# Kernel optimization log

Measured on AMD Instinct MI355X. Metric: run time of the kernel, lower is better.

Reference implementation:

```python
import jax, jax.numpy as jnp
import numpy as np

V, E, H, M = 256, 512, 512, 128
D = 2 * H  # decoder hidden
B, L_TXT, T_MEL = 32, 256, 800
EPS = 1e-5


def setup_inputs() -> dict:
    key = jax.random.key(0)
    ks = jax.random.split(key, 24)
    s = 0.02
    inp = {
        'x': jax.random.randint(ks[0], (B, L_TXT), 0, V),
        'text_seq_lens': jax.random.randint(ks[1], (B,), 1, L_TXT + 1),
        'y': jax.random.normal(ks[2], (B, T_MEL, M), jnp.float32),
        'mel_spec_lens': jax.random.randint(ks[3], (B,), 1, T_MEL + 1),
        'emb': jax.random.normal(ks[4], (V, E)) * s,
        'conv1_w': jax.random.normal(ks[5], (E, E, 3)) * s,
        'conv1_b': jnp.zeros((E,)),
        'bn1_g': jnp.ones((E,)), 'bn1_b': jnp.zeros((E,)),
        'conv2_w': jax.random.normal(ks[6], (E, E, 3)) * s,
        'conv2_b': jnp.zeros((E,)),
        'bn2_g': jnp.ones((E,)), 'bn2_b': jnp.zeros((E,)),
        'wih_f': jax.random.normal(ks[7], (4 * H, E)) * s,
        'whh_f': jax.random.normal(ks[8], (4 * H, H)) * s,
        'bih_f': jnp.zeros((4 * H,)), 'bhh_f': jnp.zeros((4 * H,)),
        'wih_b': jax.random.normal(ks[9], (4 * H, E)) * s,
        'whh_b': jax.random.normal(ks[10], (4 * H, H)) * s,
        'bih_b': jnp.zeros((4 * H,)), 'bhh_b': jnp.zeros((4 * H,)),
        'dwih': jax.random.normal(ks[11], (4 * D, M)) * s,
        'dwhh': jax.random.normal(ks[12], (4 * D, D)) * s,
        'dbih': jnp.zeros((4 * D,)), 'dbhh': jnp.zeros((4 * D,)),
        'proj_w': jax.random.normal(ks[13], (M, D)) * s,
        'proj_b': jnp.zeros((M,)),
        'gate_w': jax.random.normal(ks[14], (1, D)) * s,
        'gate_b': jnp.zeros((1,)),
    }
    return inp


def _conv_bn_relu(x, w, b, g, beta):
    # x: (B, E, L); training-mode BatchNorm (batch statistics, biased var)
    x = jax.lax.conv_general_dilated(x, w, (1,), [(1, 1)],
                                     dimension_numbers=('NCH', 'OIH', 'NCH')) + b[None, :, None]
    mu = jnp.mean(x, axis=(0, 2), keepdims=True)
    var = jnp.mean((x - mu) ** 2, axis=(0, 2), keepdims=True)
    x = (x - mu) * jax.lax.rsqrt(var + EPS) * g[None, :, None] + beta[None, :, None]
    return jax.nn.relu(x)


def _lstm_last(xseq, lens, wih, whh, bih, bhh):
    # Run LSTM over full padded seq, freezing state past each length.
    # Returns final (h, c) == state at t = len-1 (packed-sequence semantics).
    Bb, T, _ = xseq.shape
    Hh = whh.shape[1]
    pre = jnp.einsum('bte,ge->btg', xseq, wih) + bih + bhh  # (B,T,4H)

    def step(carry, inp):
        h, c = carry
        xt, t = inp
        gates = xt + h @ whh.T
        i, f, g, o = jnp.split(gates, 4, axis=-1)
        c_n = jax.nn.sigmoid(f) * c + jax.nn.sigmoid(i) * jnp.tanh(g)
        h_n = jax.nn.sigmoid(o) * jnp.tanh(c_n)
        valid = (t < lens)[:, None]
        return (jnp.where(valid, h_n, h), jnp.where(valid, c_n, c)), None

    init = (jnp.zeros((Bb, Hh), xseq.dtype), jnp.zeros((Bb, Hh), xseq.dtype))
    (h, c), _ = jax.lax.scan(step, init, (pre.transpose(1, 0, 2), jnp.arange(T)))
    return h, c


def _forward(x, text_seq_lens, y, mel_spec_lens, emb, conv1_w, conv1_b, bn1_g, bn1_b,
             conv2_w, conv2_b, bn2_g, bn2_b, wih_f, whh_f, bih_f, bhh_f,
             wih_b, whh_b, bih_b, bhh_b, dwih, dwhh, dbih, dbhh,
             proj_w, proj_b, gate_w, gate_b):
    xe = emb[x]                       # (B, L, E)
    h = xe.transpose(0, 2, 1)         # (B, E, L)
    h = _conv_bn_relu(h, conv1_w, conv1_b, bn1_g, bn1_b)  # dropout = identity (eval)
    h = _conv_bn_relu(h, conv2_w, conv2_b, bn2_g, bn2_b)
    h = h.transpose(0, 2, 1)          # (B, L, E)

    # bidirectional encoder LSTM final states (packed semantics)
    hf, cf = _lstm_last(h, text_seq_lens, wih_f, whh_f, bih_f, bhh_f)
    # reverse each sequence within its valid length for the backward direction
    t_idx = jnp.arange(h.shape[1])[None, :]
    rev_idx = jnp.clip(text_seq_lens[:, None] - 1 - t_idx, 0, h.shape[1] - 1)
    h_rev = jnp.take_along_axis(h, rev_idx[:, :, None], axis=1)
    hb, cb = _lstm_last(h_rev, text_seq_lens, wih_b, whh_b, bih_b, bhh_b)

    hid = jnp.concatenate([hf, hb], axis=1)  # (B, 2H)
    cel = jnp.concatenate([cf, cb], axis=1)

    Tm = y.shape[1]

    def dec_step(carry, _):
        hd, cd, inp = carry
        gates = inp @ dwih.T + dbih + dbhh + hd @ dwhh.T
        i, f, g, o = jnp.split(gates, 4, axis=-1)
        cd = jax.nn.sigmoid(f) * cd + jax.nn.sigmoid(i) * jnp.tanh(g)
        hd = jax.nn.sigmoid(o) * jnp.tanh(cd)
        mel = hd @ proj_w.T + proj_b          # (B, M)
        gate = hd @ gate_w.T + gate_b         # (B, 1)
        return (hd, cd, mel), (mel, gate[:, 0])

    sos = jnp.zeros((y.shape[0], M), y.dtype)
    _, (mels, gates) = jax.lax.scan(dec_step, (hid, cel, sos), None, length=Tm)
    mel_outputs = mels.transpose(1, 0, 2)     # (B, Tm, M)
    gate_outputs = gates.T                    # (B, Tm)

    mask = jnp.arange(Tm)[None, :] > mel_spec_lens[:, None]  # (B, Tm), strictly >
    masked_mel = jnp.where(mask[:, :, None], 0.0, mel_outputs)
    masked_gate = jnp.where(mask, 1000.0, gate_outputs)
    return masked_mel, masked_gate, mask


def reference(x, text_seq_lens, y, mel_spec_lens, emb, conv1_w, conv1_b, bn1_g, bn1_b,
              conv2_w, conv2_b, bn2_g, bn2_b, wih_f, whh_f, bih_f, bhh_f,
              wih_b, whh_b, bih_b, bhh_b, dwih, dwhh, dbih, dbhh,
              proj_w, proj_b, gate_w, gate_b):
    return _forward(x, text_seq_lens, y, mel_spec_lens, emb, conv1_w, conv1_b,
                    bn1_g, bn1_b, conv2_w, conv2_b, bn2_g, bn2_b,
                    wih_f, whh_f, bih_f, bhh_f, wih_b, whh_b, bih_b, bhh_b,
                    dwih, dwhh, dbih, dbhh, proj_w, proj_b, gate_w, gate_b)
```

## Files before the change

kernel.cpp:

```cpp
#include <hip/hip_runtime.h>


typedef float f4 __attribute__((ext_vector_type(4)));
typedef _Float16 h8 __attribute__((ext_vector_type(8)));
typedef _Float16 half_t;
typedef unsigned long long u64;

#define B_    32
#define LTXT  256
#define TMEL  800
#define EE    512
#define HH    512
#define DD    1024
#define MM    128
#define NROWS 8192
#define GATE_OFF 3276800
#define MASK_OFF 3302400

#define RING_D 801
#define RING_E 257
#define HOP    13

#define WS_MBE        0ull
#define WS_MBD        16384ull
#define WS_HENC       49152ull
#define WS_ZERO_BYTES 114688ull
#define WS_HD         16891904ull
#define WS_BUFX       69386240ull
#define WS_BUFY       77774848ull
#define WS_CONVF      86163456ull
#define WS_WEFF       86163456ull
#define WS_W0         94552064ull
#define WS_WP1        102940672ull
#define WS_WP2        104513536ull
#define WS_WIHP       106086400ull
#define WS_WHHP       110280704ull
#define WS_BSUM       114475008ull
#define WS_BEFF       114491392ull
#define WS_B0         114507776ull
#define WS_MEAN       114524160ull
#define WS_RSTD       114526208ull
#define WS_PROJW      114528256ull
#define WS_PROJG      114790400ull
#define WS_CEL        114823168ull

__device__ __forceinline__ float sigm(float x) { return 1.f / (1.f + __expf(-x)); }
__device__ __forceinline__ float tanh_f(float x) {
    float e = __expf(2.f * x);
    return 1.f - 2.f / (e + 1.f);
}

__device__ __forceinline__ void st_atom64(void* p, u64 v) {
    asm volatile("global_atomic_swap_x2 %0, %1, off" :: "v"(p), "v"(v) : "memory");
}
__device__ __forceinline__ void st_atom32(unsigned* p, unsigned v) {
    asm volatile("global_atomic_swap %0, %1, off" :: "v"(p), "v"(v) : "memory");
}


__global__ void k_embed(const int* __restrict__ x, const float* __restrict__ emb,
                        half_t* __restrict__ out) {
    int row = blockIdx.x;
    int tok = x[row];
    const float* e = emb + (size_t)tok * EE;
    half_t* o = out + (size_t)row * EE;
    for (int c = threadIdx.x; c < EE; c += blockDim.x) o[c] = (half_t)e[c];
}

__global__ void k_packconvw(const float* __restrict__ w, half_t* __restrict__ wp) {
    int idx = blockIdx.x * 256 + threadIdx.x;
    if (idx >= 3 * EE * EE) return;
    int s = idx / (EE * EE);
    int rem = idx - s * EE * EE;
    int eo = rem >> 9, ei = rem & 511;
    wp[idx] = (half_t)w[(size_t)eo * (EE * 3) + ei * 3 + s];
}

__global__ __launch_bounds__(256) void k_conv(const half_t* __restrict__ A,
                                              const half_t* __restrict__ Wp,
                                              const float* __restrict__ bias,
                                              float* __restrict__ out) {
    const int nt = blockIdx.x, et = blockIdx.y;
    const int tid = threadIdx.x;
    const int wv = tid >> 6, l = tid & 63, quad = l >> 4, lo = l & 15;
    const int rowA = nt * 64 + wv * 16 + lo;
    const int eo = et * 16 + lo;
    f4 acc = {0.f, 0.f, 0.f, 0.f};
    for (int s = 0; s < 3; ++s) {
        int lsp = (rowA & 255) + s - 1;
        bool valid = (lsp >= 0) && (lsp < 256);
        int rs = rowA + s - 1;
        rs = rs < 0 ? 0 : (rs > NROWS - 1 ? NROWS - 1 : rs);
        const half_t* ab = A + (size_t)rs * EE;
        const half_t* wb = Wp + ((size_t)s * EE + eo) * EE;
#pragma unroll 4
        for (int ks = 0; ks < 16; ++ks) {
            h8 a = {0, 0, 0, 0, 0, 0, 0, 0};
            if (valid) a = *(const h8*)(ab + ks * 32 + quad * 8);
            h8 b = *(const h8*)(wb + ks * 32 + quad * 8);
            acc = __builtin_amdgcn_mfma_f32_16x16x32_f16(a, b, acc, 0, 0, 0);
        }
    }
    const int orow = nt * 64 + wv * 16 + quad * 4;
    const float bv = bias[eo];
#pragma unroll
    for (int r = 0; r < 4; ++r) out[(size_t)(orow + r) * EE + eo] = acc[r] + bv;
}

__global__ __launch_bounds__(256) void k_bnstats(const float* __restrict__ x,
                                                 float* __restrict__ mean,
                                                 float* __restrict__ rstd) {
    const int c = blockIdx.x;
    float s = 0.f, ss = 0.f;
    for (int n = threadIdx.x; n < NROWS; n += 256) {
        float v = x[(size_t)n * EE + c];
        s += v; ss += v * v;
    }
#pragma unroll
    for (int off = 32; off > 0; off >>= 1) { s += __shfl_down(s, off); ss += __shfl_down(ss, off); }
    __shared__ float as[4], ass[4];
    int wv = threadIdx.x >> 6;
    if ((threadIdx.x & 63) == 0) { as[wv] = s; ass[wv] = ss; }
    __syncthreads();
    if (threadIdx.x == 0) {
        float S = as[0] + as[1] + as[2] + as[3];
        float SS = ass[0] + ass[1] + ass[2] + ass[3];
        float m = S / (float)NROWS;
        float var = SS / (float)NROWS - m * m;
        mean[c] = m;
        rstd[c] = rsqrtf(var + 1e-5f);
    }
}

__global__ void k_bnapply(const float* __restrict__ x, const float* __restrict__ mean,
                          const float* __restrict__ rstd, const float* __restrict__ g,
                          const float* __restrict__ beta, half_t* __restrict__ out) {
    int idx = blockIdx.x * 256 + threadIdx.x;
    if (idx >= NROWS * EE) return;
    int c = idx & (EE - 1);
    float v = (x[idx] - mean[c]) * rstd[c] * g[c] + beta[c];
    out[idx] = (half_t)(v > 0.f ? v : 0.f);
}

__global__ void k_packrec(const float* __restrict__ src, half_t* __restrict__ dst,
                          int Hdim, int kshift, int total) {
    int idx = blockIdx.x * 256 + threadIdx.x;
    if (idx >= total) return;
    int p = idx >> kshift;
    int k = idx & ((1 << kshift) - 1);
    int he = p >> 2, g = p & 3;
    dst[idx] = (half_t)src[((size_t)g * Hdim + he) * (size_t)(1 << kshift) + k];
}

__global__ void k_bsumenc(const float* __restrict__ bf, const float* __restrict__ bhf,
                          const float* __restrict__ bb, const float* __restrict__ bhb,
                          float* __restrict__ bsum) {
    int p = blockIdx.x * 256 + threadIdx.x;
    if (p >= 4096) return;
    int dir = p >> 11, pp = p & 2047;
    int he = pp >> 2, g = pp & 3;
    int row = g * HH + he;
    bsum[p] = dir ? (bb[row] + bhb[row]) : (bf[row] + bhf[row]);
}

__global__ __launch_bounds__(256) void k_weff(const float* __restrict__ dwhh,
                                              const float* __restrict__ dwih,
                                              const float* __restrict__ projw,
                                              half_t* __restrict__ weff,
                                              half_t* __restrict__ w0) {
    int row = blockIdx.x;
    int k = blockIdx.y * 256 + threadIdx.x;
    float v = dwhh[(size_t)row * DD + k];
    float acc = v;
    for (int m = 0; m < MM; ++m) acc += dwih[(size_t)row * MM + m] * projw[(size_t)m * DD + k];
    int p = ((row & (DD - 1)) << 2) | (row >> 10);
    weff[(size_t)p * DD + k] = (half_t)acc;
    w0[(size_t)p * DD + k] = (half_t)v;
}

__global__ void k_bdec(const float* __restrict__ dbih, const float* __restrict__ dbhh,
                       const float* __restrict__ dwih, const float* __restrict__ projb,
                       float* __restrict__ beff, float* __restrict__ b0) {
    int p = blockIdx.x * 256 + threadIdx.x;
    if (p >= 4096) return;
    int he = p >> 2, g = p & 3;
    int row = g * DD + he;
    float bb = dbih[row] + dbhh[row];
    float acc = bb;
    for (int m = 0; m < MM; ++m) acc += dwih[(size_t)row * MM + m] * projb[m];
    b0[p] = bb;
    beff[p] = acc;
}

__global__ void k_cast(const float* __restrict__ src, half_t* __restrict__ dst, int n) {
    int idx = blockIdx.x * 256 + threadIdx.x;
    if (idx < n) dst[idx] = (half_t)src[idx];
}

__global__ void k_projg(const float* __restrict__ gw, half_t* __restrict__ pg) {
    int idx = blockIdx.x * 256 + threadIdx.x;
    if (idx >= 16 * DD) return;
    int row = idx >> 10, k = idx & (DD - 1);
    pg[idx] = (half_t)(row == 0 ? gw[k] : 0.f);
}

__global__ void k_mask(const int* __restrict__ lens, float* __restrict__ out) {
    int idx = blockIdx.x * 256 + threadIdx.x;
    if (idx >= B_ * TMEL) return;
    int b = idx / TMEL, t = idx - b * TMEL;
    out[MASK_OFF + idx] = (t > lens[b]) ? 1.f : 0.f;
}

__global__ __launch_bounds__(512) void k_enc(const half_t* __restrict__ X,
                                             const half_t* __restrict__ wihp,
                                             const half_t* __restrict__ whhp,
                                             const float* __restrict__ bsum,
                                             const int* __restrict__ lens,
                                             half_t* __restrict__ henc,
                                             half_t* __restrict__ hd,
                                             float* __restrict__ cel,
                                             unsigned* __restrict__ mbE) {
    const int j = blockIdx.x;
    const int d = j >> 4, jj = j & 15;
    const int dir = d >> 1, bg = d & 1;
    const int tid = threadIdx.x;
    const int wv = tid >> 6, l = tid & 63, quad = l >> 4, lo = l & 15;
    const int ue = tid >> 4;
    const int ub = tid & 15;

    __shared__ half_t s_hd[16 * 520];
    __shared__ float s_g[16][129];
    __shared__ float s_c[32][16];
    __shared__ float s_h[32][16];
    __shared__ half_t s_hh[32][16];
    __shared__ int s_len[16];

    if (tid < 16) s_len[tid] = lens[bg * 16 + tid];
    s_c[ue][ub] = 0.f;
    s_h[ue][ub] = 0.f;

    const int pr = dir * 2048 + jj * 128 + wv * 16 + lo;
    const half_t* wih_b = wihp + (size_t)pr * 512;
    const half_t* whh_b = whhp + (size_t)pr * 512;
    const float bias_n = bsum[pr];

    h8 wihreg[16], whhreg[16];
#pragma unroll
    for (int ks = 0; ks < 16; ++ks) {
        wihreg[ks] = *(const h8*)(wih_b + ks * 32 + quad * 8);
        whhreg[ks] = *(const h8*)(whh_b + ks * 32 + quad * 8);
    }

    int sp = 0, sn = HOP;
    __syncthreads();

    for (int t = 0; t < 256; ++t) {
        if (t > 0) {
            if (wv == 1 && l < 16) {
                const unsigned want = (unsigned)t;
                const unsigned* fp = mbE + (size_t)(d * 16 + jj) * 64 + l;
                while (__hip_atomic_load(fp, __ATOMIC_RELAXED, __HIP_MEMORY_SCOPE_AGENT) < want)
                    __builtin_amdgcn_s_sleep(1);
            }
            __syncthreads();
        }

        const half_t* src = henc + ((size_t)sp * 4 + d) * 8192;
        h8 tmp0 = *(const h8*)(src + (size_t)(tid + 0 * 512) * 8);
        h8 tmp1 = *(const h8*)(src + (size_t)(tid + 1 * 512) * 8);

        const int lb = s_len[lo];
        int tt = (dir == 0) ? t : (lb - 1 - t);
        tt = tt < 0 ? 0 : tt;
        const half_t* xr = X + ((size_t)(bg * 16 + lo) * 256 + tt) * 512;
        f4 accA = {0.f, 0.f, 0.f, 0.f}, accB = {0.f, 0.f, 0.f, 0.f};
#pragma unroll
        for (int ks = 0; ks < 16; ++ks) {
            h8 a = *(const h8*)(xr + ks * 32 + quad * 8);
            accA = __builtin_amdgcn_mfma_f32_16x16x32_f16(a, wihreg[ks], accA, 0, 0, 0);
        }

        {
            int c0 = tid;
            *(h8*)(s_hd + (size_t)(c0 >> 6) * 520 + (c0 & 63) * 8) = tmp0;
            int c1 = tid + 512;
            *(h8*)(s_hd + (size_t)(c1 >> 6) * 520 + (c1 & 63) * 8) = tmp1;
        }
        __syncthreads();

        const half_t* ar = s_hd + (size_t)lo * 520 + quad * 8;
#pragma unroll
        for (int ks = 0; ks < 16; ++ks) {
            h8 a = *(const h8*)(ar + ks * 32);
            accB = __builtin_amdgcn_mfma_f32_16x16x32_f16(a, whhreg[ks], accB, 0, 0, 0);
        }
#pragma unroll
        for (int r = 0; r < 4; ++r) s_g[quad * 4 + r][wv * 16 + lo] = accA[r] + accB[r] + bias_n;
        __syncthreads();
        {
            float gi = s_g[ub][ue * 4 + 0], gf = s_g[ub][ue * 4 + 1];
            float gg = s_g[ub][ue * 4 + 2], go = s_g[ub][ue * 4 + 3];
            float cn = sigm(gf) * s_c[ue][ub] + sigm(gi) * tanh_f(gg);
            float hn = sigm(go) * tanh_f(cn);
            if (t < s_len[ub]) { s_c[ue][ub] = cn; s_h[ue][ub] = hn; }
            s_hh[ue][ub] = (half_t)s_h[ue][ub];
        }
        __syncthreads();
        if (tid < 64 && t < 255) {
            int b2 = tid >> 2, e8 = (tid & 3) * 8;
            union { half_t h[8]; u64 u[2]; } pk;
#pragma unroll
            for (int i = 0; i < 8; ++i) pk.h[i] = s_hh[e8 + i][b2];
            half_t* dst = henc + ((size_t)sn * 4 + d) * 8192 + (size_t)b2 * 512 + jj * 32 + e8;
            st_atom64(dst, pk.u[0]);
            st_atom64(dst + 4, pk.u[1]);
            asm volatile("s_waitcnt vmcnt(0)");
            if (tid < 16)
                st_atom32(mbE + ((size_t)(d * 16 + tid) * 64 + jj), (unsigned)(t + 1));
        }
        if (t < 255) { sp = sn; sn += HOP; if (sn >= RING_E) sn -= RING_E; }
    }
    hd[(size_t)bg * ((size_t)RING_D * 16384) + (size_t)ub * 1024
       + dir * 512 + jj * 32 + ue] = (half_t)s_h[ue][ub];
    cel[(size_t)(bg * 16 + ub) * 1024 + dir * 512 + jj * 32 + ue] = s_c[ue][ub];
}

__global__ __launch_bounds__(512) void k_dec(const half_t* __restrict__ Weff,
                                             const half_t* __restrict__ W0,
                                             const float* __restrict__ beff,
                                             const float* __restrict__ b0,
                                             const half_t* __restrict__ projwb,
                                             const half_t* __restrict__ projg,
                                             const float* __restrict__ projb,
                                             const float* __restrict__ gateb,
                                             const int* __restrict__ mlens,
                                             const float* __restrict__ cel,
                                             half_t* __restrict__ hd,
                                             float* __restrict__ out,
                                             unsigned* __restrict__ mbD) {
    const int j = blockIdx.x;
    const int tid = threadIdx.x;
    const int wv = tid >> 6, l = tid & 63, quad = l >> 4, lo = l & 15;

    __shared__ half_t s_hd[16 * 1032];
    __shared__ float s_g[16][129];
    __shared__ float s_c[32][16];
    __shared__ half_t s_hh[32][16];
    __shared__ int s_len[32];

    if (j < 64) {
        const int g = j >> 5, jj = j & 31;
        half_t* hdG = hd + (size_t)g * ((size_t)RING_D * 16384);
        unsigned* mbG = mbD + (size_t)g * 34 * 64;
        const int ue = tid >> 4;
        const int ub = tid & 15;

        s_c[ue][ub] = cel[(size_t)(g * 16 + ub) * 1024 + jj * 32 + ue];
        const int pr = jj * 128 + wv * 16 + lo;
        const float biasE = beff[pr], bias0 = b0[pr];
        const half_t* wbE = Weff + (size_t)pr * 1024;
        const half_t* wb0 = W0 + (size_t)pr * 1024;

        h8 wreg[32];
#pragma unroll
        for (int ks = 0; ks < 32; ++ks)
            wreg[ks] = *(const h8*)(wbE + ks * 32 + quad * 8);

        int sp = 0, sn = HOP;
        __syncthreads();

        for (int t = 1; t <= TMEL; ++t) {
            if (t > 1) {
                if (tid >= 64 && tid < 96) {
                    const unsigned want = (unsigned)(t - 1);
                    const unsigned* fp = mbG + (size_t)jj * 64 + (tid - 64);
                    while (__hip_atomic_load(fp, __ATOMIC_RELAXED, __HIP_MEMORY_SCOPE_AGENT) < want)
                        __builtin_amdgcn_s_sleep(1);
                }
                __syncthreads();
            }

            {
                const half_t* src = hdG + (size_t)sp * 16384;
                h8 tp[4];
#pragma unroll
                for (int i = 0; i < 4; ++i)
                    tp[i] = *(const h8*)(src + (size_t)(tid + i * 512) * 8);
#pragma unroll
                for (int i = 0; i < 4; ++i) {
                    int c = tid + i * 512;
                    *(h8*)(s_hd + (size_t)(c >> 7) * 1032 + (c & 127) * 8) = tp[i];
                }
            }
            __syncthreads();

            const half_t* ar = s_hd + (size_t)lo * 1032 + quad * 8;
            f4 acc = {0.f, 0.f, 0.f, 0.f}, acc2 = {0.f, 0.f, 0.f, 0.f};
            if (t == 1) {
#pragma unroll 8
                for (int ks = 0; ks < 32; ks += 2) {
                    h8 a0 = *(const h8*)(ar + ks * 32);
                    h8 a1 = *(const h8*)(ar + ks * 32 + 32);
                    acc = __builtin_amdgcn_mfma_f32_16x16x32_f16(a0, *(const h8*)(wb0 + ks * 32 + quad * 8), acc, 0, 0, 0);
                    acc2 = __builtin_amdgcn_mfma_f32_16x16x32_f16(a1, *(const h8*)(wb0 + ks * 32 + 32 + quad * 8), acc2, 0, 0, 0);
                }
            } else {
#pragma unroll
                for (int ks = 0; ks < 32; ks += 2) {
                    h8 a0 = *(const h8*)(ar + ks * 32);
                    h8 a1 = *(const h8*)(ar + ks * 32 + 32);
                    acc = __builtin_amdgcn_mfma_f32_16x16x32_f16(a0, wreg[ks], acc, 0, 0, 0);
                    acc2 = __builtin_amdgcn_mfma_f32_16x16x32_f16(a1, wreg[ks + 1], acc2, 0, 0, 0);
                }
            }
            const float bn = (t == 1) ? bias0 : biasE;
#pragma unroll
            for (int r = 0; r < 4; ++r) s_g[quad * 4 + r][wv * 16 + lo] = acc[r] + acc2[r] + bn;
            __syncthreads();
            {
                float gi = s_g[ub][ue * 4 + 0], gf = s_g[ub][ue * 4 + 1];
                float gg = s_g[ub][ue * 4 + 2], go = s_g[ub][ue * 4 + 3];
                float cn = sigm(gf) * s_c[ue][ub] + sigm(gi) * tanh_f(gg);
                s_c[ue][ub] = cn;
                s_hh[ue][ub] = (half_t)(sigm(go) * tanh_f(cn));
            }
            __syncthreads();
            if (tid < 64) {
                int b2 = tid >> 2, e8 = (tid & 3) * 8;
                union { half_t h[8]; u64 u[2]; } pk;
#pragma unroll
                for (int i = 0; i < 8; ++i) pk.h[i] = s_hh[e8 + i][b2];
                half_t* dst = hdG + (size_t)sn * 16384 + (size_t)b2 * 1024 + jj * 32 + e8;
                st_atom64(dst, pk.u[0]);
                st_atom64(dst + 4, pk.u[1]);
                asm volatile("s_waitcnt vmcnt(0)");
                if (tid < 34)
                    st_atom32(mbG + ((size_t)tid * 64 + jj), (unsigned)t);
            }
            sp = sn; sn += HOP; if (sn >= RING_D) sn -= RING_D;
        }
    } else {
        const int p = j - 64;
        const int g = p >> 1;
        const bool meld = ((p & 1) == 0);
        half_t* hdG = hd + (size_t)g * ((size_t)RING_D * 16384);
        unsigned* mbG = mbD + (size_t)g * 34 * 64;
        const int cons = meld ? 32 : 33;
        const bool duty = meld || (wv == 0);
        const half_t* pw = meld ? (projwb + (size_t)(wv * 16 + lo) * 1024)
                                : (projg + (size_t)lo * 1024);
        const float biasP = meld ? projb[wv * 16 + lo] : gateb[0];

        h8 pwreg[32];
        if (duty) {
#pragma unroll
            for (int ks = 0; ks < 32; ++ks)
                pwreg[ks] = *(const h8*)(pw + ks * 32 + quad * 8);
        }
        if (tid < 32) s_len[tid] = mlens[tid];

        int spP = HOP;
        __syncthreads();

        for (int t = 1; t <= TMEL; ++t) {
            if (tid < 32) {
                const unsigned want = (unsigned)t;
                const unsigned* fp = mbG + (size_t)cons * 64 + tid;
                while (__hip_atomic_load(fp, __ATOMIC_RELAXED, __HIP_MEMORY_SCOPE_AGENT) < want)
                    __builtin_amdgcn_s_sleep(1);
            }
            __syncthreads();

            {
                const half_t* src = hdG + (size_t)spP * 16384;
                h8 tp[4];
#pragma unroll
                for (int i = 0; i < 4; ++i)
                    tp[i] = *(const h8*)(src + (size_t)(tid + i * 512) * 8);
#pragma unroll
                for (int i = 0; i < 4; ++i) {
                    int c = tid + i * 512;
                    *(h8*)(s_hd + (size_t)(c >> 7) * 1032 + (c & 127) * 8) = tp[i];
                }
            }
            __syncthreads();

            if (duty) {
                const half_t* ar = s_hd + (size_t)lo * 1032 + quad * 8;
                f4 accm = {0.f, 0.f, 0.f, 0.f}, accm2 = {0.f, 0.f, 0.f, 0.f};
#pragma unroll
                for (int ks = 0; ks < 32; ks += 2) {
                    h8 a0 = *(const h8*)(ar + ks * 32);
                    h8 a1 = *(const h8*)(ar + ks * 32 + 32);
                    accm = __builtin_amdgcn_mfma_f32_16x16x32_f16(a0, pwreg[ks], accm, 0, 0, 0);
                    accm2 = __builtin_amdgcn_mfma_f32_16x16x32_f16(a1, pwreg[ks + 1], accm2, 0, 0, 0);
                }
                accm[0] += accm2[0]; accm[1] += accm2[1];
                accm[2] += accm2[2]; accm[3] += accm2[3];
                const int pos = t - 1;
                if (meld) {
#pragma unroll
                    for (int r = 0; r < 4; ++r) {
                        int b = g * 16 + quad * 4 + r;
                        float v = accm[r] + biasP;
                        if (pos > s_len[b]) v = 0.f;
                        __builtin_nontemporal_store(v,
                            &out[(size_t)b * (TMEL * MM) + (size_t)pos * MM + wv * 16 + lo]);
                    }
                } else if (lo == 0) {
#pragma unroll
                    for (int r = 0; r < 4; ++r) {
                        int b = g * 16 + quad * 4 + r;
                        float v = accm[r] + biasP;
                        if (pos > s_len[b]) v = 1000.f;
                        __builtin_nontemporal_store(v, &out[GATE_OFF + (size_t)b * TMEL + pos]);
                    }
                }
            }
            __syncthreads();
            spP += HOP; if (spP >= RING_D) spP -= RING_D;
        }
    }
}


extern "C" void kernel_launch(void* const* d_in, const int* in_sizes, int n_in,
                              void* d_out, int out_size, void* d_ws, size_t ws_size,
                              hipStream_t stream) {
    const int* x = (const int*)d_in[0];
    const int* tlens = (const int*)d_in[1];
    const int* mlens = (const int*)d_in[3];
    const float* emb = (const float*)d_in[4];
    const float* c1w = (const float*)d_in[5];
    const float* c1b = (const float*)d_in[6];
    const float* bn1g = (const float*)d_in[7];
    const float* bn1b = (const float*)d_in[8];
    const float* c2w = (const float*)d_in[9];
    const float* c2b = (const float*)d_in[10];
    const float* bn2g = (const float*)d_in[11];
    const float* bn2b = (const float*)d_in[12];
    const float* wihf = (const float*)d_in[13];
    const float* whhf = (const float*)d_in[14];
    const float* bihf = (const float*)d_in[15];
    const float* bhhf = (const float*)d_in[16];
    const float* wihb = (const float*)d_in[17];
    const float* whhb = (const float*)d_in[18];
    const float* bihb = (const float*)d_in[19];
    const float* bhhb = (const float*)d_in[20];
    const float* dwih = (const float*)d_in[21];
    const float* dwhh = (const float*)d_in[22];
    const float* dbih = (const float*)d_in[23];
    const float* dbhh = (const float*)d_in[24];
    const float* projw = (const float*)d_in[25];
    const float* projb = (const float*)d_in[26];
    const float* gatew = (const float*)d_in[27];
    const float* gateb = (const float*)d_in[28];
    float* out = (float*)d_out;
    char* ws = (char*)d_ws;

    unsigned* mbE = (unsigned*)(ws + WS_MBE);
    unsigned* mbD = (unsigned*)(ws + WS_MBD);
    half_t* henc = (half_t*)(ws + WS_HENC);
    half_t* hd = (half_t*)(ws + WS_HD);
    half_t* bufX = (half_t*)(ws + WS_BUFX);
    half_t* bufY = (half_t*)(ws + WS_BUFY);
    float* convf = (float*)(ws + WS_CONVF);
    half_t* weff = (half_t*)(ws + WS_WEFF);
    half_t* w0 = (half_t*)(ws + WS_W0);
    half_t* wp1 = (half_t*)(ws + WS_WP1);
    half_t* wp2 = (half_t*)(ws + WS_WP2);
    float* meanb = (float*)(ws + WS_MEAN);
    float* rstdb = (float*)(ws + WS_RSTD);
    half_t* wihp = (half_t*)(ws + WS_WIHP);
    half_t* whhp = (half_t*)(ws + WS_WHHP);
    float* bsum = (float*)(ws + WS_BSUM);
    float* beff = (float*)(ws + WS_BEFF);
    float* b0 = (float*)(ws + WS_B0);
    half_t* projwb = (half_t*)(ws + WS_PROJW);
    half_t* projg = (half_t*)(ws + WS_PROJG);
    float* cel = (float*)(ws + WS_CEL);

    hipMemsetAsync(d_ws, 0, (size_t)WS_ZERO_BYTES, stream);

    k_embed<<<NROWS, 256, 0, stream>>>(x, emb, bufX);
    k_packconvw<<<(3 * EE * EE + 255) / 256, 256, 0, stream>>>(c1w, wp1);
    k_conv<<<dim3(128, 32), 256, 0, stream>>>(bufX, wp1, c1b, convf);
    k_bnstats<<<EE, 256, 0, stream>>>(convf, meanb, rstdb);
    k_bnapply<<<(NROWS * EE) / 256, 256, 0, stream>>>(convf, meanb, rstdb, bn1g, bn1b, bufY);
    k_packconvw<<<(3 * EE * EE + 255) / 256, 256, 0, stream>>>(c2w, wp2);
    k_conv<<<dim3(128, 32), 256, 0, stream>>>(bufY, wp2, c2b, convf);
    k_bnstats<<<EE, 256, 0, stream>>>(convf, meanb, rstdb);
    k_bnapply<<<(NROWS * EE) / 256, 256, 0, stream>>>(convf, meanb, rstdb, bn2g, bn2b, bufX);

    const int encTot = 2048 * 512;
    k_packrec<<<(encTot + 255) / 256, 256, 0, stream>>>(wihf, wihp, HH, 9, encTot);
    k_packrec<<<(encTot + 255) / 256, 256, 0, stream>>>(wihb, wihp + encTot, HH, 9, encTot);
    k_packrec<<<(encTot + 255) / 256, 256, 0, stream>>>(whhf, whhp, HH, 9, encTot);
    k_packrec<<<(encTot + 255) / 256, 256, 0, stream>>>(whhb, whhp + encTot, HH, 9, encTot);
    k_bsumenc<<<16, 256, 0, stream>>>(bihf, bhhf, bihb, bhhb, bsum);

    k_enc<<<64, 512, 0, stream>>>(bufX, wihp, whhp, bsum, tlens, henc, hd, cel, mbE);

    k_weff<<<dim3(4096, 4), 256, 0, stream>>>(dwhh, dwih, projw, weff, w0);
    k_bdec<<<16, 256, 0, stream>>>(dbih, dbhh, dwih, projb, beff, b0);
    k_cast<<<(MM * DD + 255) / 256, 256, 0, stream>>>(projw, projwb, MM * DD);
    k_projg<<<(16 * DD + 255) / 256, 256, 0, stream>>>(gatew, projg);

    k_dec<<<68, 512, 0, stream>>>(weff, w0, beff, b0, projwb, projg, projb, gateb,
                                  mlens, cel, hd, out, mbD);

    k_mask<<<(B_ * TMEL + 255) / 256, 256, 0, stream>>>(mlens, out);

    (void)in_sizes; (void)n_in; (void)out_size; (void)ws_size;
}
```

Before: 4.464 ms.

## Fuse encoder, decoder and weight prep into one persistent kernel with counters

```diff
diff --git a/kernel.cpp b/kernel.cpp
--- a/kernel.cpp
+++ b/kernel.cpp
@@ -20,9 +20,13 @@
 #define RING_D 801
 #define RING_E 257
 #define HOP    13
+#define ENCTOT 1048576
+#define PREPN  60
+#define ENCN   64
 
 #define WS_MBE        0ull
 #define WS_MBD        16384ull
+#define WS_CNT        40960ull
 #define WS_HENC       49152ull
 #define WS_ZERO_BYTES 114688ull
 #define WS_HD         16891904ull
@@ -53,8 +57,14 @@
 __device__ __forceinline__ void st_atom64(void* p, u64 v) {
     asm volatile("global_atomic_swap_x2 %0, %1, off" :: "v"(p), "v"(v) : "memory");
 }
-__device__ __forceinline__ void st_atom32(unsigned* p, unsigned v) {
+__device__ __forceinline__ void st_atom32(void* p, unsigned v) {
     asm volatile("global_atomic_swap %0, %1, off" :: "v"(p), "v"(v) : "memory");
+}
+__device__ __forceinline__ void st_wt32(void* p, unsigned v) {
+    asm volatile("global_store_dword %0, %1, off sc0 sc1" :: "v"(p), "v"(v) : "memory");
+}
+__device__ __forceinline__ unsigned f2u(float f) {
+    union { float f; unsigned u; } c; c.f = f; return c.u;
 }
 
 
@@ -142,214 +152,251 @@
     out[idx] = (half_t)(v > 0.f ? v : 0.f);
 }
 
-__global__ void k_packrec(const float* __restrict__ src, half_t* __restrict__ dst,
-                          int Hdim, int kshift, int total) {
-    int idx = blockIdx.x * 256 + threadIdx.x;
-    if (idx >= total) return;
-    int p = idx >> kshift;
-    int k = idx & ((1 << kshift) - 1);
-    int he = p >> 2, g = p & 3;
-    dst[idx] = (half_t)src[((size_t)g * Hdim + he) * (size_t)(1 << kshift) + k];
-}
-
-__global__ void k_bsumenc(const float* __restrict__ bf, const float* __restrict__ bhf,
-                          const float* __restrict__ bb, const float* __restrict__ bhb,
-                          float* __restrict__ bsum) {
-    int p = blockIdx.x * 256 + threadIdx.x;
-    if (p >= 4096) return;
-    int dir = p >> 11, pp = p & 2047;
-    int he = pp >> 2, g = pp & 3;
-    int row = g * HH + he;
-    bsum[p] = dir ? (bb[row] + bhb[row]) : (bf[row] + bhf[row]);
-}
-
-__global__ __launch_bounds__(256) void k_weff(const float* __restrict__ dwhh,
-                                              const float* __restrict__ dwih,
-                                              const float* __restrict__ projw,
-                                              half_t* __restrict__ weff,
-                                              half_t* __restrict__ w0) {
-    int row = blockIdx.x;
-    int k = blockIdx.y * 256 + threadIdx.x;
-    float v = dwhh[(size_t)row * DD + k];
-    float acc = v;
-    for (int m = 0; m < MM; ++m) acc += dwih[(size_t)row * MM + m] * projw[(size_t)m * DD + k];
-    int p = ((row & (DD - 1)) << 2) | (row >> 10);
-    weff[(size_t)p * DD + k] = (half_t)acc;
-    w0[(size_t)p * DD + k] = (half_t)v;
-}
-
-__global__ void k_bdec(const float* __restrict__ dbih, const float* __restrict__ dbhh,
-                       const float* __restrict__ dwih, const float* __restrict__ projb,
-                       float* __restrict__ beff, float* __restrict__ b0) {
-    int p = blockIdx.x * 256 + threadIdx.x;
-    if (p >= 4096) return;
-    int he = p >> 2, g = p & 3;
-    int row = g * DD + he;
-    float bb = dbih[row] + dbhh[row];
-    float acc = bb;
-    for (int m = 0; m < MM; ++m) acc += dwih[(size_t)row * MM + m] * projb[m];
-    b0[p] = bb;
-    beff[p] = acc;
-}
-
-__global__ void k_cast(const float* __restrict__ src, half_t* __restrict__ dst, int n) {
-    int idx = blockIdx.x * 256 + threadIdx.x;
-    if (idx < n) dst[idx] = (half_t)src[idx];
-}
-
-__global__ void k_projg(const float* __restrict__ gw, half_t* __restrict__ pg) {
-    int idx = blockIdx.x * 256 + threadIdx.x;
-    if (idx >= 16 * DD) return;
-    int row = idx >> 10, k = idx & (DD - 1);
-    pg[idx] = (half_t)(row == 0 ? gw[k] : 0.f);
-}
-
-__global__ void k_mask(const int* __restrict__ lens, float* __restrict__ out) {
-    int idx = blockIdx.x * 256 + threadIdx.x;
-    if (idx >= B_ * TMEL) return;
-    int b = idx / TMEL, t = idx - b * TMEL;
-    out[MASK_OFF + idx] = (t > lens[b]) ? 1.f : 0.f;
-}
-
-__global__ __launch_bounds__(512) void k_enc(const half_t* __restrict__ X,
-                                             const half_t* __restrict__ wihp,
-                                             const half_t* __restrict__ whhp,
-                                             const float* __restrict__ bsum,
-                                             const int* __restrict__ lens,
-                                             half_t* __restrict__ henc,
-                                             half_t* __restrict__ hd,
-                                             float* __restrict__ cel,
-                                             unsigned* __restrict__ mbE) {
-    const int j = blockIdx.x;
-    const int d = j >> 4, jj = j & 15;
-    const int dir = d >> 1, bg = d & 1;
-    const int tid = threadIdx.x;
-    const int wv = tid >> 6, l = tid & 63, quad = l >> 4, lo = l & 15;
-    const int ue = tid >> 4;
-    const int ub = tid & 15;
-
-    __shared__ half_t s_hd[16 * 520];
-    __shared__ float s_g[16][129];
-    __shared__ float s_c[32][16];
-    __shared__ float s_h[32][16];
-    __shared__ half_t s_hh[32][16];
-    __shared__ int s_len[16];
-
-    if (tid < 16) s_len[tid] = lens[bg * 16 + tid];
-    s_c[ue][ub] = 0.f;
-    s_h[ue][ub] = 0.f;
-
-    const int pr = dir * 2048 + jj * 128 + wv * 16 + lo;
-    const half_t* wih_b = wihp + (size_t)pr * 512;
-    const half_t* whh_b = whhp + (size_t)pr * 512;
-    const float bias_n = bsum[pr];
-
-    h8 wihreg[16], whhreg[16];
-#pragma unroll
-    for (int ks = 0; ks < 16; ++ks) {
-        wihreg[ks] = *(const h8*)(wih_b + ks * 32 + quad * 8);
-        whhreg[ks] = *(const h8*)(whh_b + ks * 32 + quad * 8);
-    }
-
-    int sp = 0, sn = HOP;
-    __syncthreads();
-
-    for (int t = 0; t < 256; ++t) {
-        if (t > 0) {
-            if (wv == 1 && l < 16) {
-                const unsigned want = (unsigned)t;
-                const unsigned* fp = mbE + (size_t)(d * 16 + jj) * 64 + l;
-                while (__hip_atomic_load(fp, __ATOMIC_RELAXED, __HIP_MEMORY_SCOPE_AGENT) < want)
-                    __builtin_amdgcn_s_sleep(1);
-            }
-            __syncthreads();
-        }
-
-        const half_t* src = henc + ((size_t)sp * 4 + d) * 8192;
-        h8 tmp0 = *(const h8*)(src + (size_t)(tid + 0 * 512) * 8);
-        h8 tmp1 = *(const h8*)(src + (size_t)(tid + 1 * 512) * 8);
-
-        const int lb = s_len[lo];
-        int tt = (dir == 0) ? t : (lb - 1 - t);
-        tt = tt < 0 ? 0 : tt;
-        const half_t* xr = X + ((size_t)(bg * 16 + lo) * 256 + tt) * 512;
-        f4 accA = {0.f, 0.f, 0.f, 0.f}, accB = {0.f, 0.f, 0.f, 0.f};
-#pragma unroll
-        for (int ks = 0; ks < 16; ++ks) {
-            h8 a = *(const h8*)(xr + ks * 32 + quad * 8);
-            accA = __builtin_amdgcn_mfma_f32_16x16x32_f16(a, wihreg[ks], accA, 0, 0, 0);
-        }
-
-        {
-            int c0 = tid;
-            *(h8*)(s_hd + (size_t)(c0 >> 6) * 520 + (c0 & 63) * 8) = tmp0;
-            int c1 = tid + 512;
-            *(h8*)(s_hd + (size_t)(c1 >> 6) * 520 + (c1 & 63) * 8) = tmp1;
-        }
-        __syncthreads();
-
-        const half_t* ar = s_hd + (size_t)lo * 520 + quad * 8;
-#pragma unroll
-        for (int ks = 0; ks < 16; ++ks) {
-            h8 a = *(const h8*)(ar + ks * 32);
-            accB = __builtin_amdgcn_mfma_f32_16x16x32_f16(a, whhreg[ks], accB, 0, 0, 0);
-        }
-#pragma unroll
-        for (int r = 0; r < 4; ++r) s_g[quad * 4 + r][wv * 16 + lo] = accA[r] + accB[r] + bias_n;
-        __syncthreads();
-        {
-            float gi = s_g[ub][ue * 4 + 0], gf = s_g[ub][ue * 4 + 1];
-            float gg = s_g[ub][ue * 4 + 2], go = s_g[ub][ue * 4 + 3];
-            float cn = sigm(gf) * s_c[ue][ub] + sigm(gi) * tanh_f(gg);
-            float hn = sigm(go) * tanh_f(cn);
-            if (t < s_len[ub]) { s_c[ue][ub] = cn; s_h[ue][ub] = hn; }
-            s_hh[ue][ub] = (half_t)s_h[ue][ub];
-        }
-        __syncthreads();
-        if (tid < 64 && t < 255) {
-            int b2 = tid >> 2, e8 = (tid & 3) * 8;
-            union { half_t h[8]; u64 u[2]; } pk;
-#pragma unroll
-            for (int i = 0; i < 8; ++i) pk.h[i] = s_hh[e8 + i][b2];
-            half_t* dst = henc + ((size_t)sn * 4 + d) * 8192 + (size_t)b2 * 512 + jj * 32 + e8;
-            st_atom64(dst, pk.u[0]);
-            st_atom64(dst + 4, pk.u[1]);
-            asm volatile("s_waitcnt vmcnt(0)");
-            if (tid < 16)
-                st_atom32(mbE + ((size_t)(d * 16 + tid) * 64 + jj), (unsigned)(t + 1));
-        }
-        if (t < 255) { sp = sn; sn += HOP; if (sn >= RING_E) sn -= RING_E; }
-    }
-    hd[(size_t)bg * ((size_t)RING_D * 16384) + (size_t)ub * 1024
-       + dir * 512 + jj * 32 + ue] = (half_t)s_h[ue][ub];
-    cel[(size_t)(bg * 16 + ub) * 1024 + dir * 512 + jj * 32 + ue] = s_c[ue][ub];
-}
-
-__global__ __launch_bounds__(512) void k_dec(const half_t* __restrict__ Weff,
-                                             const half_t* __restrict__ W0,
-                                             const float* __restrict__ beff,
-                                             const float* __restrict__ b0,
-                                             const half_t* __restrict__ projwb,
-                                             const half_t* __restrict__ projg,
-                                             const float* __restrict__ projb,
-                                             const float* __restrict__ gateb,
-                                             const int* __restrict__ mlens,
-                                             const float* __restrict__ cel,
-                                             half_t* __restrict__ hd,
-                                             float* __restrict__ out,
-                                             unsigned* __restrict__ mbD) {
+__global__ __launch_bounds__(512) void k_fused(
+        const float* __restrict__ wihf, const float* __restrict__ whhf,
+        const float* __restrict__ bihf, const float* __restrict__ bhhf,
+        const float* __restrict__ wihb, const float* __restrict__ whhb,
+        const float* __restrict__ bihb, const float* __restrict__ bhhb,
+        const float* __restrict__ dwih, const float* __restrict__ dwhh,
+        const float* __restrict__ dbih, const float* __restrict__ dbhh,
+        const float* __restrict__ projw, const float* __restrict__ projb,
+        const float* __restrict__ gatew, const float* __restrict__ gateb,
+        const int* __restrict__ tlens, const int* __restrict__ mlens,
+        char* __restrict__ ws, float* __restrict__ out) {
     const int j = blockIdx.x;
     const int tid = threadIdx.x;
     const int wv = tid >> 6, l = tid & 63, quad = l >> 4, lo = l & 15;
 
-    __shared__ half_t s_hd[16 * 1032];
-    __shared__ float s_g[16][129];
-    __shared__ float s_c[32][16];
-    __shared__ half_t s_hh[32][16];
-    __shared__ int s_len[32];
+    unsigned* mbE = (unsigned*)(ws + WS_MBE);
+    unsigned* mbD = (unsigned*)(ws + WS_MBD);
+    unsigned* cnt = (unsigned*)(ws + WS_CNT);
+    half_t* henc = (half_t*)(ws + WS_HENC);
+    half_t* hd = (half_t*)(ws + WS_HD);
+    half_t* X = (half_t*)(ws + WS_BUFX);
+    half_t* wihp = (half_t*)(ws + WS_WIHP);
+    half_t* whhp = (half_t*)(ws + WS_WHHP);
+    float* bsum = (float*)(ws + WS_BSUM);
+    half_t* weff = (half_t*)(ws + WS_WEFF);
+    half_t* w0 = (half_t*)(ws + WS_W0);
+    float* beff = (float*)(ws + WS_BEFF);
+    float* b0 = (float*)(ws + WS_B0);
+    half_t* projwb = (half_t*)(ws + WS_PROJW);
+    half_t* projg = (half_t*)(ws + WS_PROJG);
+    float* cel = (float*)(ws + WS_CEL);
+
+    __shared__ __align__(16) char smem[44544];
+
+    if (j >= 132) {
+        const int nthr = PREPN * 512;
+        const int gtid = (j - 132) * 512 + tid;
+        for (int a = 0; a < 4; ++a) {
+            const float* src = (a == 0) ? wihf : (a == 1) ? wihb : (a == 2) ? whhf : whhb;
+            half_t* dst = (a < 2) ? (wihp + (size_t)a * ENCTOT) : (whhp + (size_t)(a - 2) * ENCTOT);
+            for (int pr2 = gtid; pr2 < ENCTOT / 2; pr2 += nthr) {
+                int p = pr2 >> 8, k0 = (pr2 & 255) * 2;
+                int he = p >> 2, g = p & 3;
+                const float* s2 = src + ((size_t)(g * HH + he)) * 512 + k0;
+                union { half_t h[2]; unsigned u; } pk;
+                pk.h[0] = (half_t)s2[0]; pk.h[1] = (half_t)s2[1];
+                st_wt32(dst + (size_t)p * 512 + k0, pk.u);
+            }
+        }
+        for (int p = gtid; p < 4096; p += nthr) {
+            int dir = p >> 11, pp = p & 2047, he = pp >> 2, g = pp & 3;
+            int row = g * HH + he;
+            float v = dir ? (bihb[row] + bhhb[row]) : (bihf[row] + bhhf[row]);
+            st_wt32(bsum + p, f2u(v));
+        }
+        asm volatile("s_waitcnt vmcnt(0)" ::: "memory");
+        if (tid == 0)
+            __hip_atomic_fetch_add(cnt + 0, 1u, __ATOMIC_RELAXED, __HIP_MEMORY_SCOPE_AGENT);
+        for (int pr2 = gtid; pr2 < (4096 * 1024) / 2; pr2 += nthr) {
+            int row = pr2 >> 9, k0 = (pr2 & 511) * 2;
+            float v0 = dwhh[(size_t)row * DD + k0], v1 = dwhh[(size_t)row * DD + k0 + 1];
+            float a0 = v0, a1 = v1;
+            const float* dwr = dwih + (size_t)row * MM;
+            for (int m = 0; m < MM; ++m) {
+                float dw = dwr[m];
+                a0 += dw * projw[(size_t)m * DD + k0];
+                a1 += dw * projw[(size_t)m * DD + k0 + 1];
+            }
+            int p = ((row & (DD - 1)) << 2) | (row >> 10);
+            union { half_t h[2]; unsigned u; } pk;
+            pk.h[0] = (half_t)a0; pk.h[1] = (half_t)a1;
+            st_wt32(weff + (size_t)p * DD + k0, pk.u);
+            pk.h[0] = (half_t)v0; pk.h[1] = (half_t)v1;
+            st_wt32(w0 + (size_t)p * DD + k0, pk.u);
+        }
+        for (int p = gtid; p < 4096; p += nthr) {
+            int he = p >> 2, g = p & 3;
+            int row = g * DD + he;
+            float bb = dbih[row] + dbhh[row];
+            float acc = bb;
+            const float* dwr = dwih + (size_t)row * MM;
+            for (int m = 0; m < MM; ++m) acc += dwr[m] * projb[m];
+            st_wt32(b0 + p, f2u(bb));
+            st_wt32(beff + p, f2u(acc));
+        }
+        for (int i2 = gtid; i2 < (MM * DD) / 2; i2 += nthr) {
+            int i0 = 2 * i2;
+            union { half_t h[2]; unsigned u; } pk;
+            pk.h[0] = (half_t)projw[i0]; pk.h[1] = (half_t)projw[i0 + 1];
+            st_wt32(projwb + i0, pk.u);
+        }
+        for (int i2 = gtid; i2 < (16 * DD) / 2; i2 += nthr) {
+            int i0 = 2 * i2;
+            int row = i0 >> 10, k = i0 & (DD - 1);
+            union { half_t h[2]; unsigned u; } pk;
+            pk.h[0] = (half_t)(row == 0 ? gatew[k] : 0.f);
+            pk.h[1] = (half_t)(row == 0 ? gatew[k + 1] : 0.f);
+            st_wt32(projg + i0, pk.u);
+        }
+        for (int i = gtid; i < B_ * TMEL; i += nthr) {
+            int b = i / TMEL, t = i - b * TMEL;
+            __builtin_nontemporal_store((t > mlens[b]) ? 1.f : 0.f, &out[MASK_OFF + i]);
+        }
+        asm volatile("s_waitcnt vmcnt(0)" ::: "memory");
+        if (tid == 0)
+            __hip_atomic_fetch_add(cnt + 32, 1u, __ATOMIC_RELAXED, __HIP_MEMORY_SCOPE_AGENT);
+        return;
+    }
 
     if (j < 64) {
-        const int g = j >> 5, jj = j & 31;
+        if (tid == 0) {
+            while (__hip_atomic_load(cnt + 0, __ATOMIC_RELAXED, __HIP_MEMORY_SCOPE_AGENT) < (unsigned)PREPN)
+                __builtin_amdgcn_s_sleep(2);
+        }
+        __syncthreads();
+
+        const int d = j >> 4, jj = j & 15;
+        const int dir = d >> 1, bg = d & 1;
+        const int ue = tid >> 4;
+        const int ub = tid & 15;
+
+        half_t* s_hd = (half_t*)smem;
+        float (*s_g)[129] = (float(*)[129])(smem + 16640);
+        float (*s_c)[16] = (float(*)[16])(smem + 24896);
+        float (*s_h)[16] = (float(*)[16])(smem + 26944);
+        half_t (*s_hh)[16] = (half_t(*)[16])(smem + 28992);
+        int* s_len = (int*)(smem + 30016);
+
+        if (tid < 16) s_len[tid] = tlens[bg * 16 + tid];
+        s_c[ue][ub] = 0.f;
+        s_h[ue][ub] = 0.f;
+
+        const int pr = dir * 2048 + jj * 128 + wv * 16 + lo;
+        const half_t* wih_b = wihp + (size_t)pr * 512;
+        const half_t* whh_b = whhp + (size_t)pr * 512;
+        const float bias_n = bsum[pr];
+
+        h8 wihreg[16], whhreg[16];
+#pragma unroll
+        for (int ks = 0; ks < 16; ++ks) {
+            wihreg[ks] = *(const h8*)(wih_b + ks * 32 + quad * 8);
+            whhreg[ks] = *(const h8*)(whh_b + ks * 32 + quad * 8);
+        }
+
+        int sp = 0, sn = HOP;
+        __syncthreads();
+
+        for (int t = 0; t < 256; ++t) {
+            if (t > 0) {
+                if (wv == 1 && l < 16) {
+                    const unsigned want = (unsigned)t;
+                    const unsigned* fp = mbE + (size_t)(d * 16 + jj) * 64 + l;
+                    while (__hip_atomic_load(fp, __ATOMIC_RELAXED, __HIP_MEMORY_SCOPE_AGENT) < want)
+                        __builtin_amdgcn_s_sleep(1);
+                }
+                __syncthreads();
+            }
+
+            const half_t* src = henc + ((size_t)sp * 4 + d) * 8192;
+            h8 tmp0 = *(const h8*)(src + (size_t)(tid + 0 * 512) * 8);
+            h8 tmp1 = *(const h8*)(src + (size_t)(tid + 1 * 512) * 8);
+
+            const int lb = s_len[lo];
+            int tt = (dir == 0) ? t : (lb - 1 - t);
+            tt = tt < 0 ? 0 : tt;
+            const half_t* xr = X + ((size_t)(bg * 16 + lo) * 256 + tt) * 512;
+            f4 accA = {0.f, 0.f, 0.f, 0.f}, accB = {0.f, 0.f, 0.f, 0.f};
+#pragma unroll
+            for (int ks = 0; ks < 16; ++ks) {
+                h8 a = *(const h8*)(xr + ks * 32 + quad * 8);
+                accA = __builtin_amdgcn_mfma_f32_16x16x32_f16(a, wihreg[ks], accA, 0, 0, 0);
+            }
+
+            {
+                int c0 = tid;
+                *(h8*)(s_hd + (size_t)(c0 >> 6) * 520 + (c0 & 63) * 8) = tmp0;
+                int c1 = tid + 512;
+                *(h8*)(s_hd + (size_t)(c1 >> 6) * 520 + (c1 & 63) * 8) = tmp1;
+            }
+            __syncthreads();
+
+            const half_t* ar = s_hd + (size_t)lo * 520 + quad * 8;
+#pragma unroll
+            for (int ks = 0; ks < 16; ++ks) {
+                h8 a = *(const h8*)(ar + ks * 32);
+                accB = __builtin_amdgcn_mfma_f32_16x16x32_f16(a, whhreg[ks], accB, 0, 0, 0);
+            }
+#pragma unroll
+            for (int r = 0; r < 4; ++r) s_g[quad * 4 + r][wv * 16 + lo] = accA[r] + accB[r] + bias_n;
+            __syncthreads();
+            {
+                float gi = s_g[ub][ue * 4 + 0], gf = s_g[ub][ue * 4 + 1];
+                float gg = s_g[ub][ue * 4 + 2], go = s_g[ub][ue * 4 + 3];
+                float cn = sigm(gf) * s_c[ue][ub] + sigm(gi) * tanh_f(gg);
+                float hn = sigm(go) * tanh_f(cn);
+                if (t < s_len[ub]) { s_c[ue][ub] = cn; s_h[ue][ub] = hn; }
+                s_hh[ue][ub] = (half_t)s_h[ue][ub];
+            }
+            __syncthreads();
+            if (tid < 64 && t < 255) {
+                int b2 = tid >> 2, e8 = (tid & 3) * 8;
+                union { half_t h[8]; u64 u[2]; } pk;
+#pragma unroll
+                for (int i = 0; i < 8; ++i) pk.h[i] = s_hh[e8 + i][b2];
+                half_t* dst = henc + ((size_t)sn * 4 + d) * 8192 + (size_t)b2 * 512 + jj * 32 + e8;
+                st_atom64(dst, pk.u[0]);
+                st_atom64(dst + 4, pk.u[1]);
+                asm volatile("s_waitcnt vmcnt(0)");
+                if (tid < 16)
+                    st_atom32(mbE + ((size_t)(d * 16 + tid) * 64 + jj), (unsigned)(t + 1));
+            }
+            if (t < 255) { sp = sn; sn += HOP; if (sn >= RING_E) sn -= RING_E; }
+        }
+        if (!(ue & 1)) {
+            union { half_t h[2]; unsigned u; } pk;
+            pk.h[0] = (half_t)s_h[ue][ub]; pk.h[1] = (half_t)s_h[ue + 1][ub];
+            st_atom32(hd + (size_t)bg * ((size_t)RING_D * 16384) + (size_t)ub * 1024
+                      + dir * 512 + jj * 32 + ue, pk.u);
+        }
+        st_atom32(cel + (size_t)(bg * 16 + ub) * 1024 + dir * 512 + jj * 32 + ue,
+                  f2u(s_c[ue][ub]));
+        asm volatile("s_waitcnt vmcnt(0)" ::: "memory");
+        __syncthreads();
+        if (tid == 0)
+            __hip_atomic_fetch_add(cnt + 16, 1u, __ATOMIC_RELAXED, __HIP_MEMORY_SCOPE_AGENT);
+        return;
+    }
+
+    if (tid == 0) {
+        while (__hip_atomic_load(cnt + 16, __ATOMIC_RELAXED, __HIP_MEMORY_SCOPE_AGENT) < (unsigned)ENCN ||
+               __hip_atomic_load(cnt + 32, __ATOMIC_RELAXED, __HIP_MEMORY_SCOPE_AGENT) < (unsigned)PREPN)
+            __builtin_amdgcn_s_sleep(2);
+    }
+    __syncthreads();
+
+    const int dj = j - 64;
+
+    half_t* s_hd = (half_t*)smem;
+    float (*s_g)[129] = (float(*)[129])(smem + 33024);
+    float (*s_c)[16] = (float(*)[16])(smem + 41280);
+    half_t (*s_hh)[16] = (half_t(*)[16])(smem + 43328);
+    int* s_len = (int*)(smem + 44352);
+
+    if (dj < 64) {
+        const int g = dj >> 5, jj = dj & 31;
         half_t* hdG = hd + (size_t)g * ((size_t)RING_D * 16384);
         unsigned* mbG = mbD + (size_t)g * 34 * 64;
         const int ue = tid >> 4;
@@ -358,8 +405,8 @@
         s_c[ue][ub] = cel[(size_t)(g * 16 + ub) * 1024 + jj * 32 + ue];
         const int pr = jj * 128 + wv * 16 + lo;
         const float biasE = beff[pr], bias0 = b0[pr];
-        const half_t* wbE = Weff + (size_t)pr * 1024;
-        const half_t* wb0 = W0 + (size_t)pr * 1024;
+        const half_t* wbE = weff + (size_t)pr * 1024;
+        const half_t* wb0 = w0 + (size_t)pr * 1024;
 
         h8 wreg[32];
 #pragma unroll
@@ -440,7 +487,7 @@
             sp = sn; sn += HOP; if (sn >= RING_D) sn -= RING_D;
         }
     } else {
-        const int p = j - 64;
+        const int p = dj - 64;
         const int g = p >> 1;
         const bool meld = ((p & 1) == 0);
         half_t* hdG = hd + (size_t)g * ((size_t)RING_D * 16384);
@@ -558,27 +605,13 @@
     float* out = (float*)d_out;
     char* ws = (char*)d_ws;
 
-    unsigned* mbE = (unsigned*)(ws + WS_MBE);
-    unsigned* mbD = (unsigned*)(ws + WS_MBD);
-    half_t* henc = (half_t*)(ws + WS_HENC);
-    half_t* hd = (half_t*)(ws + WS_HD);
     half_t* bufX = (half_t*)(ws + WS_BUFX);
     half_t* bufY = (half_t*)(ws + WS_BUFY);
     float* convf = (float*)(ws + WS_CONVF);
-    half_t* weff = (half_t*)(ws + WS_WEFF);
-    half_t* w0 = (half_t*)(ws + WS_W0);
     half_t* wp1 = (half_t*)(ws + WS_WP1);
     half_t* wp2 = (half_t*)(ws + WS_WP2);
     float* meanb = (float*)(ws + WS_MEAN);
     float* rstdb = (float*)(ws + WS_RSTD);
-    half_t* wihp = (half_t*)(ws + WS_WIHP);
-    half_t* whhp = (half_t*)(ws + WS_WHHP);
-    float* bsum = (float*)(ws + WS_BSUM);
-    float* beff = (float*)(ws + WS_BEFF);
-    float* b0 = (float*)(ws + WS_B0);
-    half_t* projwb = (half_t*)(ws + WS_PROJW);
-    half_t* projg = (half_t*)(ws + WS_PROJG);
-    float* cel = (float*)(ws + WS_CEL);
 
     hipMemsetAsync(d_ws, 0, (size_t)WS_ZERO_BYTES, stream);
 
@@ -592,24 +625,9 @@
     k_bnstats<<<EE, 256, 0, stream>>>(convf, meanb, rstdb);
     k_bnapply<<<(NROWS * EE) / 256, 256, 0, stream>>>(convf, meanb, rstdb, bn2g, bn2b, bufX);
 
-    const int encTot = 2048 * 512;
-    k_packrec<<<(encTot + 255) / 256, 256, 0, stream>>>(wihf, wihp, HH, 9, encTot);
-    k_packrec<<<(encTot + 255) / 256, 256, 0, stream>>>(wihb, wihp + encTot, HH, 9, encTot);
-    k_packrec<<<(encTot + 255) / 256, 256, 0, stream>>>(whhf, whhp, HH, 9, encTot);
-    k_packrec<<<(encTot + 255) / 256, 256, 0, stream>>>(whhb, whhp + encTot, HH, 9, encTot);
-    k_bsumenc<<<16, 256, 0, stream>>>(bihf, bhhf, bihb, bhhb, bsum);
-
-    k_enc<<<64, 512, 0, stream>>>(bufX, wihp, whhp, bsum, tlens, henc, hd, cel, mbE);
-
-    k_weff<<<dim3(4096, 4), 256, 0, stream>>>(dwhh, dwih, projw, weff, w0);
-    k_bdec<<<16, 256, 0, stream>>>(dbih, dbhh, dwih, projb, beff, b0);
-    k_cast<<<(MM * DD + 255) / 256, 256, 0, stream>>>(projw, projwb, MM * DD);
-    k_projg<<<(16 * DD + 255) / 256, 256, 0, stream>>>(gatew, projg);
-
-    k_dec<<<68, 512, 0, stream>>>(weff, w0, beff, b0, projwb, projg, projb, gateb,
-                                  mlens, cel, hd, out, mbD);
-
-    k_mask<<<(B_ * TMEL + 255) / 256, 256, 0, stream>>>(mlens, out);
+    k_fused<<<192, 512, 0, stream>>>(wihf, whhf, bihf, bhhf, wihb, whhb, bihb, bhhb,
+                                     dwih, dwhh, dbih, dbhh, projw, projb, gatew, gateb,
+                                     tlens, mlens, ws, out);
 
     (void)in_sizes; (void)n_in; (void)out_size; (void)ws_size;
 }
```

Result: no change. 4.491 ms (+0.6%).
